# Optimization experiments

Measured on AMD Instinct MI355X. Metric: run time of the kernel, lower is better.

Reference implementation:

```python
import jax, jax.numpy as jnp
import numpy as np

N_CONST = 188
P = 16
HIDDEN = 128
DE = 5
DO = 6
N_TARGETS = 5
BATCH = 32


def _edge_indices(n):
    # receiver/sender pairs in the same order as itertools.product, skipping diagonal
    r, s = np.meshgrid(np.arange(n), np.arange(n), indexing='ij')
    mask = r != s
    return jnp.asarray(r[mask]), jnp.asarray(s[mask])  # each [n*(n-1)]


def _linear_params(key, fan_in, fan_out):
    kw, kb = jax.random.split(key)
    w = jax.random.normal(kw, (fan_in, fan_out), jnp.float32) / np.sqrt(fan_in)
    b = jax.random.normal(kb, (fan_out,), jnp.float32) * 0.01
    return w, b


def setup_inputs() -> dict:
    key = jax.random.key(0)
    ks = jax.random.split(key, 10)
    inp = {"x": jax.random.normal(ks[0], (BATCH, N_CONST, P), jnp.float32)}
    h2 = HIDDEN // 2
    dims = [
        ("fr1", 2 * P, HIDDEN), ("fr2", HIDDEN, h2), ("fr3", h2, DE),
        ("fo1", P + DE, HIDDEN), ("fo2", HIDDEN, h2), ("fo3", h2, DO),
        ("fc1", DO * N_CONST, HIDDEN), ("fc2", HIDDEN, h2), ("fc3", h2, N_TARGETS),
    ]
    for i, (name, fi, fo) in enumerate(dims):
        w, b = _linear_params(ks[i + 1], fi, fo)
        inp[name + "_w"] = w
        inp[name + "_b"] = b
    return inp


def reference(x, fr1_w, fr1_b, fr2_w, fr2_b, fr3_w, fr3_b,
              fo1_w, fo1_b, fo2_w, fo2_b, fo3_w, fo3_b,
              fc1_w, fc1_b, fc2_w, fc2_b, fc3_w, fc3_b):
    B, n, p = x.shape
    recv, send = _edge_indices(n)  # [Nr]
    # gather receiver/sender node features (replaces one-hot matmuls with Rr, Rs)
    e_in = jnp.concatenate([x[:, recv], x[:, send]], axis=-1)  # [B, Nr, 2P]
    h = jax.nn.relu(e_in @ fr1_w + fr1_b)
    h = jax.nn.relu(h @ fr2_w + fr2_b)
    E = jax.nn.relu(h @ fr3_w + fr3_b)  # [B, Nr, De]
    # scatter-add edge effects back to receiver nodes (replaces E @ Rr^T)
    Ebar = jnp.zeros((B, n, E.shape[-1]), x.dtype).at[:, recv].add(E)  # [B, N, De]
    c = jnp.concatenate([x, Ebar], axis=-1)  # [B, N, P+De]
    h = jax.nn.relu(c @ fo1_w + fo1_b)
    h = jax.nn.relu(h @ fo2_w + fo2_b)
    O = jax.nn.relu(h @ fo3_w + fo3_b)  # [B, N, Do]
    h = jax.nn.relu(O.reshape(B, -1) @ fc1_w + fc1_b)
    h = jax.nn.relu(h @ fc2_w + fc2_b)
    return h @ fc3_w + fc3_b  # [B, n_targets]
```

## Files before the change

kernel.cpp:

```cpp
#include <hip/hip_runtime.h>

#define BB   32
#define NN   188
#define PP   16
#define HID  128
#define HH2  64
#define DE   5
#define DO   6
#define NT   5
#define ROWS_O (BB*NN)
#define RTO  16
#define KO   (PP+DE)

typedef __attribute__((ext_vector_type(8))) short short8;
typedef __attribute__((ext_vector_type(4))) float float4_;
typedef __attribute__((ext_vector_type(4))) unsigned uint4_;

__device__ __forceinline__ short f2bf(float v) {
    union { float f; unsigned u; } a; a.f = v;
    unsigned r = a.u + 0x7fff + ((a.u >> 16) & 1);
    return (short)(r >> 16);
}
__device__ __forceinline__ unsigned relu_pk(float lo, float hi) {
    float l = lo > 0.f ? lo : 0.f;
    float h = hi > 0.f ? hi : 0.f;
    unsigned r;
    asm("v_cvt_pk_bf16_f32 %0, %1, %2" : "=v"(r) : "v"(l), "v"(h));
    return r;
}
__device__ __forceinline__ float4_ mfma16(short8 a, short8 b, float4_ c) {
    return __builtin_amdgcn_mfma_f32_16x16x32_bf16(a, b, c, 0, 0, 0);
}

#define XB_OFF    0
#define XB_ELTS   (BB*NN*24)
#define W1S_OFF   (XB_OFF + XB_ELTS)
#define W1S_ELTS  (8*64*8)
#define W2S_OFF   (W1S_OFF + W1S_ELTS)
#define W2S_ELTS  (16*64*8)
#define W3S_OFF   (W2S_OFF + W2S_ELTS)
#define W3S_ELTS  (2*64*8)
#define SHORT_TOTAL (W3S_OFF + W3S_ELTS)

__device__ __forceinline__ int kmap(int q, int e) {
    return (e < 4) ? (q*4 + e) : (16 + q*4 + (e - 4));
}

__global__ void prep_kernel(const float* __restrict__ x,
                            const float* __restrict__ w1,
                            const float* __restrict__ w2,
                            const float* __restrict__ w3,
                            short* __restrict__ ws)
{
    const int i = blockIdx.x * blockDim.x + threadIdx.x;
    const int stride = gridDim.x * blockDim.x;
    for (int idx = i; idx < BB*NN*PP; idx += stride) {
        int row = idx >> 4, k = idx & 15;
        ws[XB_OFF + row*24 + k] = f2bf(x[idx]);
    }
    for (int idx = i; idx < W1S_ELTS; idx += stride) {
        int t = idx >> 9;
        int l = (idx >> 3) & 63;
        int e = idx & 7;
        int q = l >> 4, n16 = l & 15;
        ws[W1S_OFF + idx] = f2bf(w1[(q*8 + e)*HID + t*16 + n16]);
    }
    for (int idx = i; idx < W2S_ELTS; idx += stride) {
        int f = idx >> 9;
        int l = (idx >> 3) & 63;
        int e = idx & 7;
        int tt = f >> 2, s = f & 3;
        int q = l >> 4, n16 = l & 15;
        int k = 32*s + kmap(q, e);
        int n = tt*16 + n16;
        ws[W2S_OFF + idx] = f2bf(w2[k*HH2 + n]);
    }
    for (int idx = i; idx < W3S_ELTS; idx += stride) {
        int s2 = idx >> 9;
        int l = (idx >> 3) & 63;
        int e = idx & 7;
        int q = l >> 4, n16 = l & 15;
        int k = 32*s2 + kmap(q, e);
        ws[W3S_OFF + idx] = (n16 < DE) ? f2bf(w3[k*DE + n16]) : (short)0;
    }
}

#define EDGE_TILE(E1C, MASKED, TI)                                              \
    {                                                                           \
        float4_ C2[4];                                                          \
        {                                                                       \
            float4_ Ca = mfma16(W1f[0], (E1C), cbv[0]);                         \
            float4_ Cb = mfma16(W1f[1], (E1C), cbv[1]);                         \
            uint4_ dv = (uint4_){ relu_pk(Ca[0], Ca[1]), relu_pk(Ca[2], Ca[3]),  \
                                  relu_pk(Cb[0], Cb[1]), relu_pk(Cb[2], Cb[3]) };\
            short8 Bf = __builtin_bit_cast(short8, dv);                         \
            C2[0] = mfma16(W2f[0],  Bf, bias2v[0]);                             \
            C2[1] = mfma16(W2f[4],  Bf, bias2v[1]);                             \
            C2[2] = mfma16(W2f[8],  Bf, bias2v[2]);                             \
            C2[3] = mfma16(W2f[12], Bf, bias2v[3]);                             \
        }                                                                       \
        _Pragma("unroll")                                                       \
        for (int s = 1; s < 4; ++s) {                                           \
            float4_ Ca = mfma16(W1f[2*s],   (E1C), cbv[2*s]);                   \
            float4_ Cb = mfma16(W1f[2*s+1], (E1C), cbv[2*s+1]);                 \
            uint4_ dv = (uint4_){ relu_pk(Ca[0], Ca[1]), relu_pk(Ca[2], Ca[3]),  \
                                  relu_pk(Cb[0], Cb[1]), relu_pk(Cb[2], Cb[3]) };\
            short8 Bf = __builtin_bit_cast(short8, dv);                         \
            C2[0] = mfma16(W2f[s],    Bf, C2[0]);                               \
            C2[1] = mfma16(W2f[4+s],  Bf, C2[1]);                               \
            C2[2] = mfma16(W2f[8+s],  Bf, C2[2]);                               \
            C2[3] = mfma16(W2f[12+s], Bf, C2[3]);                               \
        }                                                                       \
        float4_ C3;                                                             \
        {                                                                       \
            uint4_ dv = (uint4_){ relu_pk(C2[0][0], C2[0][1]), relu_pk(C2[0][2], C2[0][3]), \
                                  relu_pk(C2[1][0], C2[1][1]), relu_pk(C2[1][2], C2[1][3]) }; \
            C3 = mfma16(W3f[0], __builtin_bit_cast(short8, dv), bias3r);        \
        }                                                                       \
        {                                                                       \
            uint4_ dv = (uint4_){ relu_pk(C2[2][0], C2[2][1]), relu_pk(C2[2][2], C2[2][3]), \
                                  relu_pk(C2[3][0], C2[3][1]), relu_pk(C2[3][2], C2[3][3]) }; \
            C3 = mfma16(W3f[1], __builtin_bit_cast(short8, dv), C3);            \
        }                                                                       \
        if (MASKED) {                                                           \
            const bool ok = ((TI)*16 + n16 < NN-1);                             \
            _Pragma("unroll")                                                   \
            for (int rg = 0; rg < 4; ++rg) {                                    \
                float v = C3[rg] > 0.f ? C3[rg] : 0.f;                          \
                acc[rg] += ok ? v : 0.f;                                        \
            }                                                                   \
        } else {                                                                \
            _Pragma("unroll")                                                   \
            for (int rg = 0; rg < 4; ++rg)                                      \
                acc[rg] += C3[rg] > 0.f ? C3[rg] : 0.f;                         \
        }                                                                       \
    }

__global__ __launch_bounds__(256) __attribute__((amdgpu_waves_per_eu(2, 2)))
void edge_mfma_kernel(const short* __restrict__ ws_s,
                      const float* __restrict__ b1,
                      const float* __restrict__ b2,
                      const float* __restrict__ b3,
                      float* __restrict__ ebar)
{
    const short* xb  = ws_s + XB_OFF;
    const short* w1g = ws_s + W1S_OFF;
    const short* w2g = ws_s + W2S_OFF;
    const short* w3g = ws_s + W3S_OFF;

    const int tid  = threadIdx.x;
    const int wave = tid >> 6;
    const int lane = tid & 63;
    const int n16  = lane & 15;
    const int q    = lane >> 4;
    const int bi   = blockIdx.x * 4 + wave;
    const int b    = bi / NN;
    const int recv = bi - b*NN;

    short8 W1f[8];
    #pragma unroll
    for (int t = 0; t < 8; ++t)
        W1f[t] = *(const short8*)(w1g + t*512 + lane*8);
    short8 W2f[16];
    #pragma unroll
    for (int f = 0; f < 16; ++f)
        W2f[f] = *(const short8*)(w2g + f*512 + lane*8);
    short8 W3f[2];
    #pragma unroll
    for (int s = 0; s < 2; ++s)
        W3f[s] = *(const short8*)(w3g + s*512 + lane*8);
    float4_ cbv[8];
    #pragma unroll
    for (int t = 0; t < 8; ++t)
        cbv[t] = *(const float4_*)(b1 + t*16 + q*4);
    float4_ bias2v[4];
    #pragma unroll
    for (int tt = 0; tt < 4; ++tt)
        bias2v[tt] = *(const float4_*)(b2 + tt*16 + q*4);
    float4_ bias3r;
    #pragma unroll
    for (int rg = 0; rg < 4; ++rg) {
        int o = q*4 + rg;
        bias3r[rg] = (o < DE) ? b3[o] : 0.f;
    }

    const short* xrow = xb + b*(NN*24);
    const bool rside = (q < 2);
    const int qoff = (q & 1)*8;

    float acc[4] = {0.f, 0.f, 0.f, 0.f};

    short8 E1;
    {
        int send0 = n16 + (n16 >= recv ? 1 : 0);
        const int node = rside ? recv : send0;
        E1 = *(const short8*)(xrow + node*24 + qoff);
    }

    #pragma unroll 1
    for (int ti = 0; ti < 11; ++ti) {
        short8 E1c = E1;
        {
            int en = (ti+1)*16 + n16;
            int send = en + (en >= recv ? 1 : 0);
            if (send > NN-1) send = NN-1;
            const int node = rside ? recv : send;
            E1 = *(const short8*)(xrow + node*24 + qoff);
        }
        EDGE_TILE(E1c, false, ti)
    }
    EDGE_TILE(E1, true, 11)

    #pragma unroll
    for (int rg = 0; rg < 4; ++rg) {
        acc[rg] += __shfl_xor(acc[rg], 1);
        acc[rg] += __shfl_xor(acc[rg], 2);
        acc[rg] += __shfl_xor(acc[rg], 4);
        acc[rg] += __shfl_xor(acc[rg], 8);
    }
    if (n16 == 0) {
        #pragma unroll
        for (int rg = 0; rg < 4; ++rg) {
            int o = q*4 + rg;
            if (o < DE) ebar[bi*DE + o] = acc[rg];
        }
    }
}

__global__ __launch_bounds__(256)
void obj_mlp_kernel(const float* __restrict__ x, const float* __restrict__ ebar,
                    const float* __restrict__ w1, const float* __restrict__ b1,
                    const float* __restrict__ w2, const float* __restrict__ b2,
                    const float* __restrict__ w3, const float* __restrict__ b3,
                    float* __restrict__ o_out)
{
    __shared__ float sW[HID*HH2];
    __shared__ float sB1[HID];
    __shared__ float sB2[HH2];
    __shared__ float sCin[RTO*KO];
    __shared__ float sH1[RTO*HID];
    __shared__ float sH2t[HH2*(RTO+1)];
    const int tid = threadIdx.x;
    const int rbase = blockIdx.x * RTO;

    for (int i = tid; i < KO*HID; i += 256) sW[i] = w1[i];
    if (tid < HID) sB1[tid] = b1[tid];
    else if (tid < HID+HH2) sB2[tid-HID] = b2[tid-HID];
    for (int i = tid; i < RTO*KO; i += 256) {
        int r = i / KO, k = i - r*KO;
        int gr = rbase + r;
        int b = gr / NN;
        int node = gr - b*NN;
        sCin[i] = (k < PP) ? x[(b*NN+node)*PP + k]
                           : ebar[(b*NN+node)*DE + (k-PP)];
    }
    __syncthreads();

    {
        const int j = tid & (HID-1);
        const int g = tid >> 7;
        float w[KO];
        #pragma unroll
        for (int k = 0; k < KO; ++k) w[k] = sW[k*HID + j];
        const float bj = sB1[j];
        #pragma unroll
        for (int rr = 0; rr < 8; ++rr) {
            const int r = g*8 + rr;
            const float* e = &sCin[r*KO];
            float a0=0.f,a1=0.f,a2=0.f;
            #pragma unroll
            for (int k = 0; k < KO; k += 3) {
                a0 += w[k+0]*e[k+0];
                a1 += w[k+1]*e[k+1];
                a2 += w[k+2]*e[k+2];
            }
            float v = a0+a1+a2+bj;
            sH1[r*HID + j] = v > 0.f ? v : 0.f;
        }
    }
    __syncthreads();
    for (int i = tid; i < HID*HH2; i += 256) sW[i] = w2[i];
    __syncthreads();

    {
        const int j = tid & (HH2-1);
        const int g = tid >> 6;
        float acc[4];
        #pragma unroll
        for (int rr = 0; rr < 4; ++rr) acc[rr] = sB2[j];
        #pragma unroll
        for (int kc = 0; kc < HID; kc += 32) {
            float w[32];
            #pragma unroll
            for (int kk = 0; kk < 32; ++kk) w[kk] = sW[(kc+kk)*HH2 + j];
            #pragma unroll
            for (int rr = 0; rr < 4; ++rr) {
                const float* h = &sH1[(g*4+rr)*HID + kc];
                float a0=0.f,a1=0.f,a2=0.f,a3=0.f;
                #pragma unroll
                for (int kk = 0; kk < 32; kk += 4) {
                    a0 += w[kk+0]*h[kk+0];
                    a1 += w[kk+1]*h[kk+1];
                    a2 += w[kk+2]*h[kk+2];
                    a3 += w[kk+3]*h[kk+3];
                }
                acc[rr] += (a0+a1)+(a2+a3);
            }
        }
        #pragma unroll
        for (int rr = 0; rr < 4; ++rr) {
            float v = acc[rr];
            sH2t[j*(RTO+1) + (g*4+rr)] = v > 0.f ? v : 0.f;
        }
    }
    __syncthreads();

    if (tid < RTO*DO) {
        const int r = tid & (RTO-1);
        const int c = tid >> 4;
        float a0=0.f,a1=0.f,a2=0.f,a3=0.f;
        #pragma unroll
        for (int k = 0; k < HH2; k += 4) {
            a0 += sH2t[(k+0)*(RTO+1)+r]*w3[(k+0)*DO+c];
            a1 += sH2t[(k+1)*(RTO+1)+r]*w3[(k+1)*DO+c];
            a2 += sH2t[(k+2)*(RTO+1)+r]*w3[(k+2)*DO+c];
            a3 += sH2t[(k+3)*(RTO+1)+r]*w3[(k+3)*DO+c];
        }
        float v = (a0+a1)+(a2+a3) + b3[c];
        v = v > 0.f ? v : 0.f;
        int gr = rbase + r;
        int b = gr / NN;
        int node = gr - b*NN;
        o_out[b*(NN*DO) + node*DO + c] = v;
    }
}

__global__ __launch_bounds__(256)
void fc1_kernel(const float* __restrict__ o_in,
                const float* __restrict__ w1, const float* __restrict__ b1,
                float* __restrict__ h1_ws)
{
    __shared__ __align__(16) float s_o[NN*DO];
    __shared__ float s_red[16][17];
    const int tid = threadIdx.x;
    const int b   = blockIdx.x >> 3;
    const int cg  = blockIdx.x & 7;

    for (int i = tid; i < NN*DO; i += 256) s_o[i] = o_in[b*(NN*DO) + i];
    __syncthreads();

    const int col = tid & 15;
    const int sl  = tid >> 4;
    const int jg  = cg*16 + col;
    const int k0  = sl*71;
    const int k1  = (k0 + 71 < NN*DO) ? k0 + 71 : NN*DO;

    float a0=0.f, a1=0.f, a2=0.f, a3=0.f;
    int k = k0;
    for (; k + 3 < k1; k += 4) {
        a0 += s_o[k+0] * w1[(size_t)(k+0)*HID + jg];
        a1 += s_o[k+1] * w1[(size_t)(k+1)*HID + jg];
        a2 += s_o[k+2] * w1[(size_t)(k+2)*HID + jg];
        a3 += s_o[k+3] * w1[(size_t)(k+3)*HID + jg];
    }
    for (; k < k1; ++k)
        a0 += s_o[k] * w1[(size_t)k*HID + jg];
    s_red[col][sl] = (a0+a1)+(a2+a3);
    __syncthreads();

    if (tid < 16) {
        float t = 0.f;
        #pragma unroll
        for (int s = 0; s < 16; ++s) t += s_red[tid][s];
        t += b1[cg*16 + tid];
        h1_ws[b*HID + cg*16 + tid] = t > 0.f ? t : 0.f;
    }
}

__global__ __launch_bounds__(256)
void fc23_kernel(const float* __restrict__ h1_ws,
                 const float* __restrict__ w2, const float* __restrict__ b2,
                 const float* __restrict__ w3, const float* __restrict__ b3,
                 float* __restrict__ out)
{
    __shared__ float s_h1[HID];
    __shared__ float s_p[256];
    __shared__ float s_h2[HH2];
    const int b = blockIdx.x, tid = threadIdx.x;

    if (tid < HID) s_h1[tid] = h1_ws[b*HID + tid];
    __syncthreads();

    {
        const int j = tid & (HH2-1);
        const int q = tid >> 6;
        float acc = 0.f;
        #pragma unroll
        for (int kk = 0; kk < 32; ++kk) {
            int k = q*32 + kk;
            acc += s_h1[k] * w2[k*HH2 + j];
        }
        s_p[tid] = acc;
    }
    __syncthreads();
    if (tid < HH2) {
        float v = s_p[tid] + s_p[tid+64] + s_p[tid+128] + s_p[tid+192] + b2[tid];
        s_h2[tid] = v > 0.f ? v : 0.f;
    }
    __syncthreads();

    if (tid < NT) {
        float acc = b3[tid];
        #pragma unroll
        for (int k = 0; k < HH2; ++k)
            acc += s_h2[k] * w3[k*NT + tid];
        out[b*NT + tid] = acc;
    }
}

extern "C" void kernel_launch(void* const* d_in, const int* in_sizes, int n_in,
                              void* d_out, int out_size, void* d_ws, size_t ws_size,
                              hipStream_t stream) {
    (void)in_sizes; (void)n_in; (void)out_size; (void)ws_size;
    const float* x     = (const float*)d_in[0];
    const float* fr1_w = (const float*)d_in[1];
    const float* fr1_b = (const float*)d_in[2];
    const float* fr2_w = (const float*)d_in[3];
    const float* fr2_b = (const float*)d_in[4];
    const float* fr3_w = (const float*)d_in[5];
    const float* fr3_b = (const float*)d_in[6];
    const float* fo1_w = (const float*)d_in[7];
    const float* fo1_b = (const float*)d_in[8];
    const float* fo2_w = (const float*)d_in[9];
    const float* fo2_b = (const float*)d_in[10];
    const float* fo3_w = (const float*)d_in[11];
    const float* fo3_b = (const float*)d_in[12];
    const float* fc1_w = (const float*)d_in[13];
    const float* fc1_b = (const float*)d_in[14];
    const float* fc2_w = (const float*)d_in[15];
    const float* fc2_b = (const float*)d_in[16];
    const float* fc3_w = (const float*)d_in[17];
    const float* fc3_b = (const float*)d_in[18];

    short* ws_s = (short*)d_ws;
    size_t fbase = ((size_t)SHORT_TOTAL*2 + 15) & ~(size_t)15;
    float* ebar  = (float*)((char*)d_ws + fbase);
    float* o_ws  = ebar + BB*NN*DE;
    float* h1_ws = o_ws + BB*NN*DO;

    prep_kernel<<<128, 256, 0, stream>>>(x, fr1_w, fr2_w, fr3_w, ws_s);
    edge_mfma_kernel<<<(BB*NN)/4, 256, 0, stream>>>(ws_s, fr1_b, fr2_b, fr3_b, ebar);
    obj_mlp_kernel<<<ROWS_O/RTO, 256, 0, stream>>>(
        x, ebar, fo1_w, fo1_b, fo2_w, fo2_b, fo3_w, fo3_b, o_ws);
    fc1_kernel<<<BB*8, 256, 0, stream>>>(o_ws, fc1_w, fc1_b, h1_ws);
    fc23_kernel<<<BB, 256, 0, stream>>>(
        h1_ws, fc2_w, fc2_b, fc3_w, fc3_b, (float*)d_out);
}
```

Measured before the change: 148.9 us.

## Stage fr2 weights in LDS for occupancy and fuse fc kernels via atomic counter

The edge MLP kernel no longer keeps all 16 fr2 weight fragments in registers. It copies them into shared memory once per block and reads them from LDS inside the inner loop, and the waves-per-EU hint is relaxed from exactly 2 to at least 3, which should free VGPRs for higher occupancy. Separately, the fc1 and fc2/fc3 kernels are merged: the last of the 8 column-group blocks per batch, found through an atomic counter zeroed in prep, computes the tail. This saves one launch, but adds LDS traffic in the hot loop and a threadfence/atomic handshake.

```diff
diff --git a/kernel.cpp b/kernel.cpp
--- a/kernel.cpp
+++ b/kernel.cpp
@@ -50,10 +50,12 @@
                             const float* __restrict__ w1,
                             const float* __restrict__ w2,
                             const float* __restrict__ w3,
-                            short* __restrict__ ws)
+                            short* __restrict__ ws,
+                            int* __restrict__ cnt)
 {
     const int i = blockIdx.x * blockDim.x + threadIdx.x;
     const int stride = gridDim.x * blockDim.x;
+    if (i < BB) cnt[i] = 0;
     for (int idx = i; idx < BB*NN*PP; idx += stride) {
         int row = idx >> 4, k = idx & 15;
         ws[XB_OFF + row*24 + k] = f2bf(x[idx]);
@@ -89,27 +91,35 @@
     {                                                                           \
         float4_ C2[4];                                                          \
         {                                                                       \
+            short8 A0 = *(const short8*)(w2b + 0*512);                          \
+            short8 A1 = *(const short8*)(w2b + 4*512);                          \
+            short8 A2t = *(const short8*)(w2b + 8*512);                         \
+            short8 A3 = *(const short8*)(w2b + 12*512);                         \
             float4_ Ca = mfma16(W1f[0], (E1C), cbv[0]);                         \
             float4_ Cb = mfma16(W1f[1], (E1C), cbv[1]);                         \
             uint4_ dv = (uint4_){ relu_pk(Ca[0], Ca[1]), relu_pk(Ca[2], Ca[3]),  \
                                   relu_pk(Cb[0], Cb[1]), relu_pk(Cb[2], Cb[3]) };\
             short8 Bf = __builtin_bit_cast(short8, dv);                         \
-            C2[0] = mfma16(W2f[0],  Bf, bias2v[0]);                             \
-            C2[1] = mfma16(W2f[4],  Bf, bias2v[1]);                             \
-            C2[2] = mfma16(W2f[8],  Bf, bias2v[2]);                             \
-            C2[3] = mfma16(W2f[12], Bf, bias2v[3]);                             \
+            C2[0] = mfma16(A0,  Bf, bias2v[0]);                                 \
+            C2[1] = mfma16(A1,  Bf, bias2v[1]);                                 \
+            C2[2] = mfma16(A2t, Bf, bias2v[2]);                                 \
+            C2[3] = mfma16(A3,  Bf, bias2v[3]);                                 \
         }                                                                       \
         _Pragma("unroll")                                                       \
         for (int s = 1; s < 4; ++s) {                                           \
+            short8 A0 = *(const short8*)(w2b + (s)*512);                        \
+            short8 A1 = *(const short8*)(w2b + (4+s)*512);                      \
+            short8 A2t = *(const short8*)(w2b + (8+s)*512);                     \
+            short8 A3 = *(const short8*)(w2b + (12+s)*512);                     \
             float4_ Ca = mfma16(W1f[2*s],   (E1C), cbv[2*s]);                   \
             float4_ Cb = mfma16(W1f[2*s+1], (E1C), cbv[2*s+1]);                 \
             uint4_ dv = (uint4_){ relu_pk(Ca[0], Ca[1]), relu_pk(Ca[2], Ca[3]),  \
                                   relu_pk(Cb[0], Cb[1]), relu_pk(Cb[2], Cb[3]) };\
             short8 Bf = __builtin_bit_cast(short8, dv);                         \
-            C2[0] = mfma16(W2f[s],    Bf, C2[0]);                               \
-            C2[1] = mfma16(W2f[4+s],  Bf, C2[1]);                               \
-            C2[2] = mfma16(W2f[8+s],  Bf, C2[2]);                               \
-            C2[3] = mfma16(W2f[12+s], Bf, C2[3]);                               \
+            C2[0] = mfma16(A0,  Bf, C2[0]);                                     \
+            C2[1] = mfma16(A1,  Bf, C2[1]);                                     \
+            C2[2] = mfma16(A2t, Bf, C2[2]);                                     \
+            C2[3] = mfma16(A3,  Bf, C2[3]);                                     \
         }                                                                       \
         float4_ C3;                                                             \
         {                                                                       \
@@ -136,7 +146,7 @@
         }                                                                       \
     }
 
-__global__ __launch_bounds__(256) __attribute__((amdgpu_waves_per_eu(2, 2)))
+__global__ __launch_bounds__(256) __attribute__((amdgpu_waves_per_eu(3)))
 void edge_mfma_kernel(const short* __restrict__ ws_s,
                       const float* __restrict__ b1,
                       const float* __restrict__ b2,
@@ -145,8 +155,9 @@
 {
     const short* xb  = ws_s + XB_OFF;
     const short* w1g = ws_s + W1S_OFF;
-    const short* w2g = ws_s + W2S_OFF;
     const short* w3g = ws_s + W3S_OFF;
+
+    __shared__ __align__(16) short sW2[W2S_ELTS];
 
     const int tid  = threadIdx.x;
     const int wave = tid >> 6;
@@ -157,14 +168,17 @@
     const int b    = bi / NN;
     const int recv = bi - b*NN;
 
+    {
+        const uint4* src = (const uint4*)(ws_s + W2S_OFF);
+        uint4* dst = (uint4*)sW2;
+        #pragma unroll
+        for (int i = 0; i < 4; ++i) dst[tid + i*256] = src[tid + i*256];
+    }
+
     short8 W1f[8];
     #pragma unroll
     for (int t = 0; t < 8; ++t)
         W1f[t] = *(const short8*)(w1g + t*512 + lane*8);
-    short8 W2f[16];
-    #pragma unroll
-    for (int f = 0; f < 16; ++f)
-        W2f[f] = *(const short8*)(w2g + f*512 + lane*8);
     short8 W3f[2];
     #pragma unroll
     for (int s = 0; s < 2; ++s)
@@ -184,6 +198,9 @@
         bias3r[rg] = (o < DE) ? b3[o] : 0.f;
     }
 
+    __syncthreads();
+
+    const short* w2b = sW2 + lane*8;
     const short* xrow = xb + b*(NN*24);
     const bool rside = (q < 2);
     const int qoff = (q & 1)*8;
@@ -336,12 +353,19 @@
 }
 
 __global__ __launch_bounds__(256)
-void fc1_kernel(const float* __restrict__ o_in,
-                const float* __restrict__ w1, const float* __restrict__ b1,
-                float* __restrict__ h1_ws)
+void fc_fused_kernel(const float* __restrict__ o_in,
+                     const float* __restrict__ w1, const float* __restrict__ b1,
+                     const float* __restrict__ w2, const float* __restrict__ b2,
+                     const float* __restrict__ w3, const float* __restrict__ b3,
+                     float* __restrict__ h1_ws, int* __restrict__ cnt,
+                     float* __restrict__ out)
 {
     __shared__ __align__(16) float s_o[NN*DO];
     __shared__ float s_red[16][17];
+    __shared__ float s_h1[HID];
+    __shared__ float s_p[256];
+    __shared__ float s_h2[HH2];
+    __shared__ int s_last;
     const int tid = threadIdx.x;
     const int b   = blockIdx.x >> 3;
     const int cg  = blockIdx.x & 7;
@@ -349,23 +373,25 @@
     for (int i = tid; i < NN*DO; i += 256) s_o[i] = o_in[b*(NN*DO) + i];
     __syncthreads();
 
-    const int col = tid & 15;
-    const int sl  = tid >> 4;
-    const int jg  = cg*16 + col;
-    const int k0  = sl*71;
-    const int k1  = (k0 + 71 < NN*DO) ? k0 + 71 : NN*DO;
-
-    float a0=0.f, a1=0.f, a2=0.f, a3=0.f;
-    int k = k0;
-    for (; k + 3 < k1; k += 4) {
-        a0 += s_o[k+0] * w1[(size_t)(k+0)*HID + jg];
-        a1 += s_o[k+1] * w1[(size_t)(k+1)*HID + jg];
-        a2 += s_o[k+2] * w1[(size_t)(k+2)*HID + jg];
-        a3 += s_o[k+3] * w1[(size_t)(k+3)*HID + jg];
-    }
-    for (; k < k1; ++k)
-        a0 += s_o[k] * w1[(size_t)k*HID + jg];
-    s_red[col][sl] = (a0+a1)+(a2+a3);
+    {
+        const int col = tid & 15;
+        const int sl  = tid >> 4;
+        const int jg  = cg*16 + col;
+        const int k0  = sl*71;
+        const int k1  = (k0 + 71 < NN*DO) ? k0 + 71 : NN*DO;
+
+        float a0=0.f, a1=0.f, a2=0.f, a3=0.f;
+        int k = k0;
+        for (; k + 3 < k1; k += 4) {
+            a0 += s_o[k+0] * w1[(size_t)(k+0)*HID + jg];
+            a1 += s_o[k+1] * w1[(size_t)(k+1)*HID + jg];
+            a2 += s_o[k+2] * w1[(size_t)(k+2)*HID + jg];
+            a3 += s_o[k+3] * w1[(size_t)(k+3)*HID + jg];
+        }
+        for (; k < k1; ++k)
+            a0 += s_o[k] * w1[(size_t)k*HID + jg];
+        s_red[col][sl] = (a0+a1)+(a2+a3);
+    }
     __syncthreads();
 
     if (tid < 16) {
@@ -375,29 +401,28 @@
         t += b1[cg*16 + tid];
         h1_ws[b*HID + cg*16 + tid] = t > 0.f ? t : 0.f;
     }
-}
-
-__global__ __launch_bounds__(256)
-void fc23_kernel(const float* __restrict__ h1_ws,
-                 const float* __restrict__ w2, const float* __restrict__ b2,
-                 const float* __restrict__ w3, const float* __restrict__ b3,
-                 float* __restrict__ out)
-{
-    __shared__ float s_h1[HID];
-    __shared__ float s_p[256];
-    __shared__ float s_h2[HH2];
-    const int b = blockIdx.x, tid = threadIdx.x;
+
+    __threadfence();
+    __syncthreads();
+    if (tid == 0) {
+        int prev = __hip_atomic_fetch_add(&cnt[b], 1, __ATOMIC_ACQ_REL,
+                                          __HIP_MEMORY_SCOPE_AGENT);
+        s_last = (prev == 7) ? 1 : 0;
+    }
+    __syncthreads();
+    if (!s_last) return;
+    __threadfence();
 
     if (tid < HID) s_h1[tid] = h1_ws[b*HID + tid];
     __syncthreads();
 
     {
         const int j = tid & (HH2-1);
-        const int q = tid >> 6;
+        const int qq = tid >> 6;
         float acc = 0.f;
         #pragma unroll
         for (int kk = 0; kk < 32; ++kk) {
-            int k = q*32 + kk;
+            int k = qq*32 + kk;
             acc += s_h1[k] * w2[k*HH2 + j];
         }
         s_p[tid] = acc;
@@ -447,12 +472,12 @@
     float* ebar  = (float*)((char*)d_ws + fbase);
     float* o_ws  = ebar + BB*NN*DE;
     float* h1_ws = o_ws + BB*NN*DO;
-
-    prep_kernel<<<128, 256, 0, stream>>>(x, fr1_w, fr2_w, fr3_w, ws_s);
+    int*   cnt   = (int*)(h1_ws + BB*HID);
+
+    prep_kernel<<<128, 256, 0, stream>>>(x, fr1_w, fr2_w, fr3_w, ws_s, cnt);
     edge_mfma_kernel<<<(BB*NN)/4, 256, 0, stream>>>(ws_s, fr1_b, fr2_b, fr3_b, ebar);
     obj_mlp_kernel<<<ROWS_O/RTO, 256, 0, stream>>>(
         x, ebar, fo1_w, fo1_b, fo2_w, fo2_b, fo3_w, fo3_b, o_ws);
-    fc1_kernel<<<BB*8, 256, 0, stream>>>(o_ws, fc1_w, fc1_b, h1_ws);
-    fc23_kernel<<<BB, 256, 0, stream>>>(
-        h1_ws, fc2_w, fc2_b, fc3_w, fc3_b, (float*)d_out);
-}
+    fc_fused_kernel<<<BB*8, 256, 0, stream>>>(
+        o_ws, fc1_w, fc1_b, fc2_w, fc2_b, fc3_w, fc3_b, h1_ws, cnt, (float*)d_out);
+}
```

Result: slower. 196.4 us (+31.9%).
